# Kernel tuning notes

Measured on AMD Instinct MI355X. Metric: run time of the kernel, lower is better.

Reference implementation:

```python
import jax, jax.numpy as jnp
import numpy as np

B = 16       # graphs per batch
N = 256      # nodes per graph (Hi-C submatrix bins)
NT = B * N   # total nodes
E = 131072   # total edges
DIN = 32     # input feature dim (HYPERPARAMETERS['input_shape'])
H1, H2 = 16, 32
HID = 32     # ContactCNN hidden dim
W7 = 7       # final conv width


def setup_inputs() -> dict:
    key = jax.random.key(0)
    ks = jax.random.split(key, 16)
    x = jax.random.normal(ks[0], (NT, DIN), dtype=jnp.float32)
    edge_index = jax.random.randint(ks[1], (2, E), 0, NT, dtype=jnp.int64)
    edge_attr = jax.random.uniform(ks[2], (E,), dtype=jnp.float32)
    batch_index = jnp.repeat(jnp.arange(B, dtype=jnp.int64), N)
    s = 0.1
    params = dict(
        W0=jax.random.normal(ks[3], (DIN, H1), dtype=jnp.float32) * s,
        b0=jnp.zeros((H1,), dtype=jnp.float32),
        W1=jax.random.normal(ks[4], (H1, H2), dtype=jnp.float32) * s,
        b1=jnp.zeros((H2,), dtype=jnp.float32),
        W2=jax.random.normal(ks[5], (H2, H2), dtype=jnp.float32) * s,
        b2=jnp.zeros((H2,), dtype=jnp.float32),
        Wc=jax.random.normal(ks[6], (HID, H2), dtype=jnp.float32) * s,  # 1x1 conv: [out=HID, in=H2]
        bc=jnp.zeros((HID,), dtype=jnp.float32),
        Wp=jax.random.normal(ks[7], (1, HID, W7, W7), dtype=jnp.float32) * s,  # OIHW
        bp=jnp.zeros((1,), dtype=jnp.float32),
    )
    return dict(x=x, edge_index=edge_index, edge_attr=edge_attr,
                batch_index=batch_index, **params)


def _gcn_norm(edge_index, edge_weight, n):
    # PyG gcn_norm with improved=True (self-loop fill value 2.0)
    src, dst = edge_index[0], edge_index[1]
    loop = jnp.arange(n, dtype=src.dtype)
    src_a = jnp.concatenate([src, loop])
    dst_a = jnp.concatenate([dst, loop])
    w_a = jnp.concatenate([edge_weight, jnp.full((n,), 2.0, dtype=edge_weight.dtype)])
    deg = jax.ops.segment_sum(w_a, dst_a, num_segments=n)
    deg_safe = jnp.where(deg > 0, deg, 1.0)
    dinv = jnp.where(deg > 0, jax.lax.rsqrt(deg_safe), 0.0)
    norm = dinv[src_a] * w_a * dinv[dst_a]
    return src_a, dst_a, norm


def _gcn_layer(h, W, b, src_a, dst_a, norm, n):
    h = h @ W                                  # [n, out]
    msg = norm[:, None] * h[src_a]             # gather + scale
    return jax.ops.segment_sum(msg, dst_a, num_segments=n) + b  # scatter-add


def reference(x, edge_index, edge_attr, batch_index,
              W0, b0, W1, b1, W2, b2, Wc, bc, Wp, bp):
    n = x.shape[0]
    src_a, dst_a, norm = _gcn_norm(edge_index, edge_attr, n)
    h = jax.nn.relu(_gcn_layer(x, W0, b0, src_a, dst_a, norm, n))
    h = jax.nn.relu(_gcn_layer(h, W1, b1, src_a, dst_a, norm, n))
    h = jax.nn.relu(_gcn_layer(h, W2, b2, src_a, dst_a, norm, n))
    z = h.reshape(B, N, -1)                    # process_graph_batch
    # ContactCNN: broadcast outer product -> 1x1 conv -> ReLU -> 7x7 conv -> sigmoid
    zm = jnp.einsum('bid,bjd->bdij', z, z)     # [B, D, N, N]
    c = jax.nn.relu(jnp.einsum('bdij,hd->bhij', zm, Wc) + bc[None, :, None, None])
    s = jax.lax.conv_general_dilated(
        c, Wp, window_strides=(1, 1), padding='SAME',
        dimension_numbers=('NCHW', 'OIHW', 'NCHW')) + bp[None, :, None, None]
    return jax.nn.sigmoid(s)                   # [B, 1, N, N]
```

## Files before the change

kernel.cpp:

```cpp
#include <hip/hip_runtime.h>
#include <hip/hip_bf16.h>
#include <hip/hip_fp16.h>

#define NT 4096
#define NE 131072

#define OFF_DEG  0
#define OFF_A    16384
#define OFF_G1T  33570816
#define OFF_G2T  33701888
#define OFF_G3T  33964032
#define OFF_H3   34226176
#define OFF_W2T  34488320

typedef __attribute__((ext_vector_type(8))) short bf16x8;
typedef __attribute__((ext_vector_type(4))) float f32x4;

__device__ inline unsigned int align16(unsigned int hi, unsigned int lo) {
#if __has_builtin(__builtin_amdgcn_alignbit)
    return __builtin_amdgcn_alignbit(hi, lo, 16);
#else
    return (lo >> 16) | (hi << 16);
#endif
}

__device__ inline unsigned short bfb(float x) {
    return __hip_bfloat16_raw(__float2bfloat16(x)).x;
}

__device__ inline void atomic_add_bf16(unsigned short* base, unsigned int idx, float v) {
    unsigned long long addr = (unsigned long long)(base + (idx & ~1u));
    unsigned int bits = ((unsigned int)bfb(v)) << ((idx & 1u) * 16);
    asm volatile("global_atomic_pk_add_bf16 %0, %1, off" :: "v"(addr), "v"(bits) : "memory");
}


__global__ void k_deg(const int* __restrict__ ei, const float* __restrict__ ew,
                      float* __restrict__ deg) {
    int e = blockIdx.x * 256 + threadIdx.x;
    if (e < NE) atomicAdd(&deg[ei[NE + e]], ew[e]);
}

__global__ void k_scatter(const int* __restrict__ ei, const float* __restrict__ ew,
                          const float* __restrict__ deg, unsigned short* __restrict__ A16,
                          const float* __restrict__ x, const float* __restrict__ W0,
                          unsigned short* __restrict__ G1T,
                          const float* __restrict__ Wp, unsigned int* __restrict__ w2) {
    int e = blockIdx.x * 256 + threadIdx.x;
    if (e < NE) {
        int s = ei[e], d = ei[NE + e];
        float v = rsqrtf(deg[s] + 2.f) * ew[e] * rsqrtf(deg[d] + 2.f);
        atomic_add_bf16(A16, (unsigned int)d * 4096u + (unsigned int)s, v);
    }
    if (e < NT) {
        atomic_add_bf16(A16, (unsigned int)e * 4097u, 2.f / (deg[e] + 2.f));
    }
    if (e < NT * 16) {
        int node = e & 4095, co = e >> 12;
        const float4* xr = (const float4*)(x + node * 32);
        float a = 0.f;
        #pragma unroll
        for (int r = 0; r < 8; r++) {
            float4 f = xr[r];
            a += f.x * W0[(r*4+0)*16 + co] + f.y * W0[(r*4+1)*16 + co]
               + f.z * W0[(r*4+2)*16 + co] + f.w * W0[(r*4+3)*16 + co];
        }
        G1T[co * 4096 + node] = bfb(a);
    }
    if (e >= NE - 1568) {
        int k = e - (NE - 1568);
        __half hh = __float2half(Wp[k]);
        __half2 h2 = __halves2half2(hh, hh);
        w2[k] = *(unsigned int*)&h2;
    }
}


template <int NIN, int NOUT, bool LAST>
__global__ __launch_bounds__(512) void k_gcn(const unsigned short* __restrict__ A16,
                                             const unsigned short* __restrict__ Gt,
                                             const float* __restrict__ bias,
                                             const float* __restrict__ W,
                                             unsigned short* __restrict__ Gout) {
    constexpr int T = NIN / 16;
    __shared__ float red[8][T][16][16];
    __shared__ unsigned short wtile[16 * 40];
    int mt = blockIdx.x;
    int tid = threadIdx.x;
    int w = tid >> 6, lane = tid & 63, m = lane & 15, q = lane >> 4;
    int kw = w * 512;

    const unsigned short* arow = A16 + (size_t)(mt * 16 + m) * 4096 + kw + q * 8;
    f32x4 acc[T];
    #pragma unroll
    for (int t = 0; t < T; t++) acc[t] = (f32x4){0.f, 0.f, 0.f, 0.f};

    bf16x8 wfrag;
    if (!LAST && w < NOUT / 16) {
        #pragma unroll
        for (int j = 0; j < 8; j++) {
            int ci = q * 8 + j;
            wfrag[j] = (ci < NIN) ? (short)bfb(W[ci * NOUT + w * 16 + m]) : (short)0;
        }
    }

    #pragma unroll 4
    for (int s = 0; s < 16; s++) {
        bf16x8 bA = *(const bf16x8*)(arow + s * 32);
        #pragma unroll
        for (int t = 0; t < T; t++) {
            bf16x8 af = *(const bf16x8*)(Gt + (size_t)(t * 16 + m) * 4096 + kw + q * 8 + s * 32);
            acc[t] = __builtin_amdgcn_mfma_f32_16x16x32_bf16(af, bA, acc[t], 0, 0, 0);
        }
    }
    #pragma unroll
    for (int t = 0; t < T; t++)
        #pragma unroll
        for (int r = 0; r < 4; r++) red[w][t][q*4 + r][m] = acc[t][r];
    __syncthreads();

    if (tid < T * 256) {
        int dstp = tid & 15, cop = (tid >> 4) & 15, t = tid >> 8;
        float sum = 0.f;
        #pragma unroll
        for (int w8 = 0; w8 < 8; w8++) sum += red[w8][t][cop][dstp];
        int co = t * 16 + cop;
        float val = fmaxf(sum + bias[co], 0.f);
        if (LAST) Gout[(size_t)(mt * 16 + dstp) * 32 + co] = bfb(val);
        else      wtile[dstp * 40 + co] = bfb(val);
    }
    if (!LAST && NIN == 16 && tid >= 256 && tid < 512) {
        int idx = tid - 256;
        wtile[(idx & 15) * 40 + 16 + ((idx >> 4) & 15)] = 0;
    }
    __syncthreads();

    if (!LAST && w < NOUT / 16) {
        bf16x8 af = *(const bf16x8*)&wtile[m * 40 + q * 8];
        f32x4 o = (f32x4){0.f, 0.f, 0.f, 0.f};
        o = __builtin_amdgcn_mfma_f32_16x16x32_bf16(af, wfrag, o, 0, 0, 0);
        uint2 ov;
        ov.x = (unsigned int)bfb(o[0]) | ((unsigned int)bfb(o[1]) << 16);
        ov.y = (unsigned int)bfb(o[2]) | ((unsigned int)bfb(o[3]) << 16);
        *(uint2*)&Gout[(size_t)(w * 16 + m) * 4096 + mt * 16 + q * 4] = ov;
    }
}


__global__ __launch_bounds__(512) void k_cc(const unsigned short* __restrict__ h3,
                                            const float* __restrict__ Wc,
                                            const float* __restrict__ bc,
                                            const unsigned int* __restrict__ w2,
                                            const float* __restrict__ bp,
                                            float* __restrict__ out) {
    __shared__ unsigned short zs[256 * 40];
    __shared__ float wcs[32 * 36];
    __shared__ __align__(16) unsigned short ct[4 * 32 * 272];
    __shared__ __align__(16) unsigned short pt[4][4096];

    int band = blockIdx.x, bb = blockIdx.y;
    int i0 = band * 16;
    int tid = threadIdx.x;
    int lane = tid & 63, w = tid >> 6;
    int m = lane & 15, q = lane >> 4;

    {
        int row = tid >> 1, half = tid & 1;
        const uint4* src = (const uint4*)(h3 + (size_t)(bb * 256 + row) * 32) + half * 2;
        uint4 v0 = src[0], v1 = src[1];
        uint4* dst = (uint4*)&zs[row * 40 + half * 16];
        dst[0] = v0; dst[1] = v1;
    }
    #pragma unroll
    for (int k = tid; k < 1024; k += 512) wcs[(k >> 5) * 36 + (k & 31)] = Wc[k];
    for (int k = tid; k < 4 * 32 * 136; k += 512) ((unsigned int*)ct)[k] = 0;
    __syncthreads();

    bf16x8 bt[2];
    bool wok[2];
    #pragma unroll
    for (int nt = 0; nt < 2; nt++) {
        int r = i0 - 3 + nt * 16 + m;
        wok[nt] = (unsigned)r < 256u;
        r = r < 0 ? 0 : (r > 255 ? 255 : r);
        bt[nt] = *(const bf16x8*)&zs[r * 40 + q * 8];
    }
    float zaf[2][8];
    #pragma unroll
    for (int jt2 = 0; jt2 < 2; jt2++) {
        bf16x8 za = *(const bf16x8*)&zs[((w * 2 + jt2) * 16 + m) * 40 + q * 8];
        #pragma unroll
        for (int e = 0; e < 8; e++)
            zaf[jt2][e] = __uint_as_float(((unsigned int)(unsigned short)za[e]) << 16);
    }

    int gg = tid >> 7, tx = tid & 31, ty = (tid >> 5) & 3;
    __half2 acc[4][4];
    __half2 zh = __float2half2_rn(0.f);
    #pragma unroll
    for (int o = 0; o < 4; o++)
        #pragma unroll
        for (int p = 0; p < 4; p++) acc[o][p] = zh;

    for (int it = 0; it < 8; it++) {
        #pragma unroll
        for (int g = 0; g < 4; g++) {
            int h = it * 4 + g;
            float wf[8];
            *(float4*)&wf[0] = *(const float4*)&wcs[h * 36 + q * 8];
            *(float4*)&wf[4] = *(const float4*)&wcs[h * 36 + q * 8 + 4];
            float bch = bc[h];
            #pragma unroll
            for (int jt2 = 0; jt2 < 2; jt2++) {
                bf16x8 afv;
                #pragma unroll
                for (int e = 0; e < 8; e++) afv[e] = (short)bfb(zaf[jt2][e] * wf[e]);
                int pos = 4 + (w * 2 + jt2) * 16 + q * 4;
                #pragma unroll
                for (int nt = 0; nt < 2; nt++) {
                    f32x4 d = (f32x4){0.f, 0.f, 0.f, 0.f};
                    d = __builtin_amdgcn_mfma_f32_16x16x32_bf16(afv, bt[nt], d, 0, 0, 0);
                    if (wok[nt]) {
                        float v0 = fmaxf(d[0] + bch, 0.f);
                        float v1 = fmaxf(d[1] + bch, 0.f);
                        float v2 = fmaxf(d[2] + bch, 0.f);
                        float v3 = fmaxf(d[3] + bch, 0.f);
                        __half2 h0 = __floats2half2_rn(v0, v1);
                        __half2 h1 = __floats2half2_rn(v2, v3);
                        uint2 o2;
                        o2.x = *(unsigned int*)&h0;
                        o2.y = *(unsigned int*)&h1;
                        *(uint2*)&ct[g * 8704 + (nt * 16 + m) * 272 + pos] = o2;
                    }
                }
            }
        }
        __syncthreads();

        {
            const unsigned short* C = ct + gg * 8704;
            const __half2* wrow = (const __half2*)w2 + (it * 4 + gg) * 49;
            #pragma unroll
            for (int dr = 0; dr < 10; dr++) {
                const uint4* p4 = (const uint4*)&C[(ty * 4 + dr) * 272 + tx * 8];
                uint4 ua = p4[0], ub = p4[1];
                unsigned int E[8] = {ua.x, ua.y, ua.z, ua.w, ub.x, ub.y, ub.z, ub.w};
                unsigned int O[7];
                #pragma unroll
                for (int k = 0; k < 7; k++) O[k] = align16(E[k + 1], E[k]);
                #pragma unroll
                for (int o = 0; o < 4; o++) {
                    if (dr - o < 0 || dr - o > 6) continue;
                    int di = dr - o;
                    #pragma unroll
                    for (int dj = 0; dj < 7; dj++) {
                        __half2 wv = wrow[di * 7 + dj];
                        #pragma unroll
                        for (int pr = 0; pr < 4; pr++) {
                            int s = 2 * pr + dj + 1;
                            unsigned int pv = (s & 1) ? O[s >> 1] : E[s >> 1];
                            acc[o][pr] = __hfma2(wv, *(__half2*)&pv, acc[o][pr]);
                        }
                    }
                }
            }
        }
        __syncthreads();
    }

    #pragma unroll
    for (int o = 0; o < 4; o++) {
        uint4 v;
        v.x = *(unsigned int*)&acc[o][0];
        v.y = *(unsigned int*)&acc[o][1];
        v.z = *(unsigned int*)&acc[o][2];
        v.w = *(unsigned int*)&acc[o][3];
        *(uint4*)&pt[gg][(ty * 4 + o) * 256 + tx * 8] = v;
    }
    __syncthreads();

    {
        int base = tid * 8;
        float fs[8];
        #pragma unroll
        for (int e = 0; e < 8; e++) fs[e] = 0.f;
        #pragma unroll
        for (int g = 0; g < 4; g++) {
            uint4 v = *(const uint4*)&pt[g][base];
            unsigned int uu[4] = {v.x, v.y, v.z, v.w};
            #pragma unroll
            for (int d = 0; d < 4; d++) {
                float2 f = __half22float2(*(__half2*)&uu[d]);
                fs[2 * d] += f.x; fs[2 * d + 1] += f.y;
            }
        }
        float bpv = bp[0];
        float rs[8];
        #pragma unroll
        for (int e = 0; e < 8; e++) rs[e] = 1.0f / (1.0f + __expf(-(fs[e] + bpv)));
        int row = base >> 8, col = base & 255;
        float* op = &out[((size_t)(bb * 256) + i0 + row) * 256 + col];
        *(float4*)op = make_float4(rs[0], rs[1], rs[2], rs[3]);
        *(float4*)(op + 4) = make_float4(rs[4], rs[5], rs[6], rs[7]);
    }
}


extern "C" void kernel_launch(void* const* d_in, const int* in_sizes, int n_in,
                              void* d_out, int out_size, void* d_ws, size_t ws_size,
                              hipStream_t stream) {
    const float* x  = (const float*)d_in[0];
    const int*   ei = (const int*)d_in[1];
    const float* ew = (const float*)d_in[2];
    const float* W0 = (const float*)d_in[4];
    const float* b0 = (const float*)d_in[5];
    const float* W1 = (const float*)d_in[6];
    const float* b1 = (const float*)d_in[7];
    const float* W2 = (const float*)d_in[8];
    const float* b2 = (const float*)d_in[9];
    const float* Wc = (const float*)d_in[10];
    const float* bc = (const float*)d_in[11];
    const float* Wp = (const float*)d_in[12];
    const float* bp = (const float*)d_in[13];

    char* ws = (char*)d_ws;
    float*          deg  = (float*)(ws + OFF_DEG);
    unsigned short* A16  = (unsigned short*)(ws + OFF_A);
    unsigned short* G1T  = (unsigned short*)(ws + OFF_G1T);
    unsigned short* G2T  = (unsigned short*)(ws + OFF_G2T);
    unsigned short* G3T  = (unsigned short*)(ws + OFF_G3T);
    unsigned short* H3   = (unsigned short*)(ws + OFF_H3);
    unsigned int*   w2t  = (unsigned int*)(ws + OFF_W2T);

    (void)hipMemsetAsync(d_ws, 0, 16384 + 33554432, stream);

    k_deg    <<<NE/256, 256, 0, stream>>>(ei, ew, deg);
    k_scatter<<<NE/256, 256, 0, stream>>>(ei, ew, deg, A16, x, W0, G1T, Wp, w2t);

    k_gcn<16, 32, false><<<256, 512, 0, stream>>>(A16, G1T, b0, W1, G2T);
    k_gcn<32, 32, false><<<256, 512, 0, stream>>>(A16, G2T, b1, W2, G3T);
    k_gcn<32, 32, true> <<<256, 512, 0, stream>>>(A16, G3T, b2, nullptr, H3);

    k_cc<<<dim3(16, 16), 512, 0, stream>>>(H3, Wc, bc, w2t, bp, (float*)d_out);
}
```

Baseline: 196.5 us.

## Fuse graph-construction and GCN layers into one persistent kernel with grid barriers

Replaces the workspace memset, degree, scatter and three GCN-layer launches with a single persistent kernel of 256 blocks. Stages are separated by software grid barriers built on atomic counters, and the dense adjacency zeroing moves into the kernel itself. The aim is to remove launch gaps and the separate memset pass. In exchange it relies on all 256 blocks being co-resident, since the spin barriers otherwise deadlock, and it adds barrier latency between stages.

Result: slower. 280.8 us (+42.9%).

```diff
diff --git a/kernel.cpp b/kernel.cpp
--- a/kernel.cpp
+++ b/kernel.cpp
@@ -4,6 +4,7 @@
 
 #define NT 4096
 #define NE 131072
+#define NBLK 256
 
 #define OFF_DEG  0
 #define OFF_A    16384
@@ -12,6 +13,7 @@
 #define OFF_G3T  33964032
 #define OFF_H3   34226176
 #define OFF_W2T  34488320
+#define OFF_BAR  34496512
 
 typedef __attribute__((ext_vector_type(8))) short bf16x8;
 typedef __attribute__((ext_vector_type(4))) float f32x4;
@@ -34,59 +36,31 @@
     asm volatile("global_atomic_pk_add_bf16 %0, %1, off" :: "v"(addr), "v"(bits) : "memory");
 }
 
-
-__global__ void k_deg(const int* __restrict__ ei, const float* __restrict__ ew,
-                      float* __restrict__ deg) {
-    int e = blockIdx.x * 256 + threadIdx.x;
-    if (e < NE) atomicAdd(&deg[ei[NE + e]], ew[e]);
-}
-
-__global__ void k_scatter(const int* __restrict__ ei, const float* __restrict__ ew,
-                          const float* __restrict__ deg, unsigned short* __restrict__ A16,
-                          const float* __restrict__ x, const float* __restrict__ W0,
-                          unsigned short* __restrict__ G1T,
-                          const float* __restrict__ Wp, unsigned int* __restrict__ w2) {
-    int e = blockIdx.x * 256 + threadIdx.x;
-    if (e < NE) {
-        int s = ei[e], d = ei[NE + e];
-        float v = rsqrtf(deg[s] + 2.f) * ew[e] * rsqrtf(deg[d] + 2.f);
-        atomic_add_bf16(A16, (unsigned int)d * 4096u + (unsigned int)s, v);
-    }
-    if (e < NT) {
-        atomic_add_bf16(A16, (unsigned int)e * 4097u, 2.f / (deg[e] + 2.f));
-    }
-    if (e < NT * 16) {
-        int node = e & 4095, co = e >> 12;
-        const float4* xr = (const float4*)(x + node * 32);
-        float a = 0.f;
-        #pragma unroll
-        for (int r = 0; r < 8; r++) {
-            float4 f = xr[r];
-            a += f.x * W0[(r*4+0)*16 + co] + f.y * W0[(r*4+1)*16 + co]
-               + f.z * W0[(r*4+2)*16 + co] + f.w * W0[(r*4+3)*16 + co];
-        }
-        G1T[co * 4096 + node] = bfb(a);
-    }
-    if (e >= NE - 1568) {
-        int k = e - (NE - 1568);
-        __half hh = __float2half(Wp[k]);
-        __half2 h2 = __halves2half2(hh, hh);
-        w2[k] = *(unsigned int*)&h2;
-    }
-}
-
+__device__ inline void gbar(unsigned int* ctr) {
+    __syncthreads();
+    if (threadIdx.x == 0) {
+        __threadfence();
+        __hip_atomic_fetch_add(ctr, 1u, __ATOMIC_RELAXED, __HIP_MEMORY_SCOPE_AGENT);
+        while (__hip_atomic_load(ctr, __ATOMIC_RELAXED, __HIP_MEMORY_SCOPE_AGENT) < NBLK)
+            __builtin_amdgcn_s_sleep(2);
+        __threadfence();
+    }
+    __syncthreads();
+}
+
+struct GcnSmem {
+    float red[8][2][16][16];
+    unsigned short wtile[16 * 40];
+};
 
 template <int NIN, int NOUT, bool LAST>
-__global__ __launch_bounds__(512) void k_gcn(const unsigned short* __restrict__ A16,
-                                             const unsigned short* __restrict__ Gt,
-                                             const float* __restrict__ bias,
-                                             const float* __restrict__ W,
-                                             unsigned short* __restrict__ Gout) {
+__device__ inline void gcn_phase(GcnSmem& sm, const unsigned short* __restrict__ A16,
+                                 const unsigned short* __restrict__ Gt,
+                                 const float* __restrict__ bias,
+                                 const float* __restrict__ W,
+                                 unsigned short* __restrict__ Gout,
+                                 int mt, int tid) {
     constexpr int T = NIN / 16;
-    __shared__ float red[8][T][16][16];
-    __shared__ unsigned short wtile[16 * 40];
-    int mt = blockIdx.x;
-    int tid = threadIdx.x;
     int w = tid >> 6, lane = tid & 63, m = lane & 15, q = lane >> 4;
     int kw = w * 512;
 
@@ -116,27 +90,27 @@
     #pragma unroll
     for (int t = 0; t < T; t++)
         #pragma unroll
-        for (int r = 0; r < 4; r++) red[w][t][q*4 + r][m] = acc[t][r];
+        for (int r = 0; r < 4; r++) sm.red[w][t][q * 4 + r][m] = acc[t][r];
     __syncthreads();
 
     if (tid < T * 256) {
         int dstp = tid & 15, cop = (tid >> 4) & 15, t = tid >> 8;
         float sum = 0.f;
         #pragma unroll
-        for (int w8 = 0; w8 < 8; w8++) sum += red[w8][t][cop][dstp];
+        for (int w8 = 0; w8 < 8; w8++) sum += sm.red[w8][t][cop][dstp];
         int co = t * 16 + cop;
         float val = fmaxf(sum + bias[co], 0.f);
         if (LAST) Gout[(size_t)(mt * 16 + dstp) * 32 + co] = bfb(val);
-        else      wtile[dstp * 40 + co] = bfb(val);
+        else      sm.wtile[dstp * 40 + co] = bfb(val);
     }
     if (!LAST && NIN == 16 && tid >= 256 && tid < 512) {
         int idx = tid - 256;
-        wtile[(idx & 15) * 40 + 16 + ((idx >> 4) & 15)] = 0;
+        sm.wtile[(idx & 15) * 40 + 16 + ((idx >> 4) & 15)] = 0;
     }
     __syncthreads();
 
     if (!LAST && w < NOUT / 16) {
-        bf16x8 af = *(const bf16x8*)&wtile[m * 40 + q * 8];
+        bf16x8 af = *(const bf16x8*)&sm.wtile[m * 40 + q * 8];
         f32x4 o = (f32x4){0.f, 0.f, 0.f, 0.f};
         o = __builtin_amdgcn_mfma_f32_16x16x32_bf16(af, wfrag, o, 0, 0, 0);
         uint2 ov;
@@ -144,6 +118,75 @@
         ov.y = (unsigned int)bfb(o[2]) | ((unsigned int)bfb(o[3]) << 16);
         *(uint2*)&Gout[(size_t)(w * 16 + m) * 4096 + mt * 16 + q * 4] = ov;
     }
+    __syncthreads();
+}
+
+__global__ __launch_bounds__(512) void k_graph(
+        const int* __restrict__ ei, const float* __restrict__ ew,
+        const float* __restrict__ x, const float* __restrict__ W0,
+        const float* __restrict__ b0, const float* __restrict__ W1,
+        const float* __restrict__ b1, const float* __restrict__ W2,
+        const float* __restrict__ b2, const float* __restrict__ Wp,
+        unsigned int* __restrict__ w2, float* __restrict__ deg,
+        unsigned short* __restrict__ A16,
+        unsigned short* __restrict__ G1T, unsigned short* __restrict__ G2T,
+        unsigned short* __restrict__ G3T, unsigned short* __restrict__ H3,
+        unsigned int* __restrict__ bars) {
+    __shared__ GcnSmem sm;
+    int blk = blockIdx.x, tid = threadIdx.x;
+    int gid = blk * 512 + tid;
+
+    {
+        uint4 z4 = {0u, 0u, 0u, 0u};
+        uint4* ap = (uint4*)(A16 + (size_t)blk * 16 * 4096);
+        #pragma unroll
+        for (int k = 0; k < 16; k++) ap[tid + k * 512] = z4;
+        if (blk == 0) {
+            float4 zf = {0.f, 0.f, 0.f, 0.f};
+            float4* dp = (float4*)deg;
+            dp[tid * 2] = zf;
+            dp[tid * 2 + 1] = zf;
+        }
+    }
+    gbar(&bars[0]);
+
+    atomicAdd(&deg[ei[NE + gid]], ew[gid]);
+    gbar(&bars[1]);
+
+    {
+        int s = ei[gid], d = ei[NE + gid];
+        float v = rsqrtf(deg[s] + 2.f) * ew[gid] * rsqrtf(deg[d] + 2.f);
+        atomic_add_bf16(A16, (unsigned int)d * 4096u + (unsigned int)s, v);
+        if (gid < NT * 16) {
+            int node = gid & 4095, co = gid >> 12;
+            const float4* xr = (const float4*)(x + node * 32);
+            float a = 0.f;
+            #pragma unroll
+            for (int r = 0; r < 8; r++) {
+                float4 f = xr[r];
+                a += f.x * W0[(r*4+0)*16 + co] + f.y * W0[(r*4+1)*16 + co]
+                   + f.z * W0[(r*4+2)*16 + co] + f.w * W0[(r*4+3)*16 + co];
+            }
+            G1T[co * 4096 + node] = bfb(a);
+        }
+        if (gid >= NT * 16 && gid < NT * 16 + 1568) {
+            int k = gid - NT * 16;
+            __half hh = __float2half(Wp[k]);
+            __half2 h2 = __halves2half2(hh, hh);
+            w2[k] = *(unsigned int*)&h2;
+        }
+        if (gid >= NE - NT) {
+            int n = gid - (NE - NT);
+            atomic_add_bf16(A16, (unsigned int)n * 4097u, 2.f / (deg[n] + 2.f));
+        }
+    }
+    gbar(&bars[2]);
+
+    gcn_phase<16, 32, false>(sm, A16, G1T, b0, W1, G2T, blk, tid);
+    gbar(&bars[3]);
+    gcn_phase<32, 32, false>(sm, A16, G2T, b1, W2, G3T, blk, tid);
+    gbar(&bars[4]);
+    gcn_phase<32, 32, true >(sm, A16, G3T, b2, nullptr, H3, blk, tid);
 }
 
 
@@ -331,15 +374,11 @@
     unsigned short* G3T  = (unsigned short*)(ws + OFF_G3T);
     unsigned short* H3   = (unsigned short*)(ws + OFF_H3);
     unsigned int*   w2t  = (unsigned int*)(ws + OFF_W2T);
-
-    (void)hipMemsetAsync(d_ws, 0, 16384 + 33554432, stream);
-
-    k_deg    <<<NE/256, 256, 0, stream>>>(ei, ew, deg);
-    k_scatter<<<NE/256, 256, 0, stream>>>(ei, ew, deg, A16, x, W0, G1T, Wp, w2t);
-
-    k_gcn<16, 32, false><<<256, 512, 0, stream>>>(A16, G1T, b0, W1, G2T);
-    k_gcn<32, 32, false><<<256, 512, 0, stream>>>(A16, G2T, b1, W2, G3T);
-    k_gcn<32, 32, true> <<<256, 512, 0, stream>>>(A16, G3T, b2, nullptr, H3);
-
+    unsigned int*   bars = (unsigned int*)(ws + OFF_BAR);
+
+    (void)hipMemsetAsync(bars, 0, 64, stream);
+
+    k_graph<<<NBLK, 512, 0, stream>>>(ei, ew, x, W0, b0, W1, b1, W2, b2,
+                                      Wp, w2t, deg, A16, G1T, G2T, G3T, H3, bars);
     k_cc<<<dim3(16, 16), 512, 0, stream>>>(H3, Wc, bc, w2t, bp, (float*)d_out);
 }
```

## Halve contact-CNN row bands and fuse A16 zeroing into degree kernel

Applied to the files above, without the earlier changes.

The contact-CNN kernel now covers 8 output rows per block instead of 16. The grid doubles to 512 blocks, shared buffers shrink and a launch-bounds occupancy hint is added, with each thread now holding a single output row of accumulators. This trades more recomputation of the 7x7 halo rows (the 1x1 conv runs over 16 padded rows for every 8 outputs) for more blocks and higher occupancy on the GPU. Separately, the 32 MB memset of the dense adjacency is folded into the degree atomic kernel as vectorized stores, leaving only a small memset for the degree array.

After: 206.6 us. 5.1% more time.

```diff
diff --git a/kernel.cpp b/kernel.cpp
--- a/kernel.cpp
+++ b/kernel.cpp
@@ -35,10 +35,17 @@
 }
 
 
-__global__ void k_deg(const int* __restrict__ ei, const float* __restrict__ ew,
-                      float* __restrict__ deg) {
-    int e = blockIdx.x * 256 + threadIdx.x;
-    if (e < NE) atomicAdd(&deg[ei[NE + e]], ew[e]);
+__global__ __launch_bounds__(256) void k_zerodeg(const int* __restrict__ ei,
+                                                 const float* __restrict__ ew,
+                                                 float* __restrict__ deg,
+                                                 unsigned short* __restrict__ A16) {
+    int blk = blockIdx.x, tid = threadIdx.x;
+    uint4 z4 = {0u, 0u, 0u, 0u};
+    uint4* ap = (uint4*)(A16 + (size_t)blk * 16384);
+    #pragma unroll
+    for (int k = 0; k < 8; k++) ap[tid + k * 256] = z4;
+    int gid = blk * 256 + tid;
+    if (gid < NE) atomicAdd(&deg[ei[NE + gid]], ew[gid]);
 }
 
 __global__ void k_scatter(const int* __restrict__ ei, const float* __restrict__ ew,
@@ -147,19 +154,19 @@
 }
 
 
-__global__ __launch_bounds__(512) void k_cc(const unsigned short* __restrict__ h3,
-                                            const float* __restrict__ Wc,
-                                            const float* __restrict__ bc,
-                                            const unsigned int* __restrict__ w2,
-                                            const float* __restrict__ bp,
-                                            float* __restrict__ out) {
+__global__ __launch_bounds__(512, 4) void k_cc(const unsigned short* __restrict__ h3,
+                                               const float* __restrict__ Wc,
+                                               const float* __restrict__ bc,
+                                               const unsigned int* __restrict__ w2,
+                                               const float* __restrict__ bp,
+                                               float* __restrict__ out) {
     __shared__ unsigned short zs[256 * 40];
     __shared__ float wcs[32 * 36];
-    __shared__ __align__(16) unsigned short ct[4 * 32 * 272];
-    __shared__ __align__(16) unsigned short pt[4][4096];
+    __shared__ __align__(16) unsigned short ct[2 * 16 * 272];
+    __shared__ __align__(16) unsigned short pt[2][2048];
 
     int band = blockIdx.x, bb = blockIdx.y;
-    int i0 = band * 16;
+    int i0 = band * 8;
     int tid = threadIdx.x;
     int lane = tid & 63, w = tid >> 6;
     int m = lane & 15, q = lane >> 4;
@@ -173,17 +180,16 @@
     }
     #pragma unroll
     for (int k = tid; k < 1024; k += 512) wcs[(k >> 5) * 36 + (k & 31)] = Wc[k];
-    for (int k = tid; k < 4 * 32 * 136; k += 512) ((unsigned int*)ct)[k] = 0;
+    for (int k = tid; k < 2 * 16 * 136; k += 512) ((unsigned int*)ct)[k] = 0;
     __syncthreads();
 
-    bf16x8 bt[2];
-    bool wok[2];
-    #pragma unroll
-    for (int nt = 0; nt < 2; nt++) {
-        int r = i0 - 3 + nt * 16 + m;
-        wok[nt] = (unsigned)r < 256u;
+    bf16x8 bt;
+    bool wok;
+    {
+        int r = i0 - 3 + m;
+        wok = (unsigned)r < 256u;
         r = r < 0 ? 0 : (r > 255 ? 255 : r);
-        bt[nt] = *(const bf16x8*)&zs[r * 40 + q * 8];
+        bt = *(const bf16x8*)&zs[r * 40 + q * 8];
     }
     float zaf[2][8];
     #pragma unroll
@@ -194,18 +200,17 @@
             zaf[jt2][e] = __uint_as_float(((unsigned int)(unsigned short)za[e]) << 16);
     }
 
-    int gg = tid >> 7, tx = tid & 31, ty = (tid >> 5) & 3;
-    __half2 acc[4][4];
+    int gg = tid >> 8, idx = tid & 255;
+    int tx = idx & 31, ty = idx >> 5;
+    __half2 acc[4];
     __half2 zh = __float2half2_rn(0.f);
     #pragma unroll
-    for (int o = 0; o < 4; o++)
-        #pragma unroll
-        for (int p = 0; p < 4; p++) acc[o][p] = zh;
-
-    for (int it = 0; it < 8; it++) {
-        #pragma unroll
-        for (int g = 0; g < 4; g++) {
-            int h = it * 4 + g;
+    for (int p = 0; p < 4; p++) acc[p] = zh;
+
+    for (int it = 0; it < 16; it++) {
+        #pragma unroll
+        for (int g = 0; g < 2; g++) {
+            int h = it * 2 + g;
             float wf[8];
             *(float4*)&wf[0] = *(const float4*)&wcs[h * 36 + q * 8];
             *(float4*)&wf[4] = *(const float4*)&wcs[h * 36 + q * 8 + 4];
@@ -216,51 +221,43 @@
                 #pragma unroll
                 for (int e = 0; e < 8; e++) afv[e] = (short)bfb(zaf[jt2][e] * wf[e]);
                 int pos = 4 + (w * 2 + jt2) * 16 + q * 4;
-                #pragma unroll
-                for (int nt = 0; nt < 2; nt++) {
-                    f32x4 d = (f32x4){0.f, 0.f, 0.f, 0.f};
-                    d = __builtin_amdgcn_mfma_f32_16x16x32_bf16(afv, bt[nt], d, 0, 0, 0);
-                    if (wok[nt]) {
-                        float v0 = fmaxf(d[0] + bch, 0.f);
-                        float v1 = fmaxf(d[1] + bch, 0.f);
-                        float v2 = fmaxf(d[2] + bch, 0.f);
-                        float v3 = fmaxf(d[3] + bch, 0.f);
-                        __half2 h0 = __floats2half2_rn(v0, v1);
-                        __half2 h1 = __floats2half2_rn(v2, v3);
-                        uint2 o2;
-                        o2.x = *(unsigned int*)&h0;
-                        o2.y = *(unsigned int*)&h1;
-                        *(uint2*)&ct[g * 8704 + (nt * 16 + m) * 272 + pos] = o2;
-                    }
+                f32x4 d = (f32x4){0.f, 0.f, 0.f, 0.f};
+                d = __builtin_amdgcn_mfma_f32_16x16x32_bf16(afv, bt, d, 0, 0, 0);
+                if (wok) {
+                    float v0 = fmaxf(d[0] + bch, 0.f);
+                    float v1 = fmaxf(d[1] + bch, 0.f);
+                    float v2 = fmaxf(d[2] + bch, 0.f);
+                    float v3 = fmaxf(d[3] + bch, 0.f);
+                    __half2 h0 = __floats2half2_rn(v0, v1);
+                    __half2 h1 = __floats2half2_rn(v2, v3);
+                    uint2 o2;
+                    o2.x = *(unsigned int*)&h0;
+                    o2.y = *(unsigned int*)&h1;
+                    *(uint2*)&ct[g * 4352 + m * 272 + pos] = o2;
                 }
             }
         }
         __syncthreads();
 
         {
-            const unsigned short* C = ct + gg * 8704;
-            const __half2* wrow = (const __half2*)w2 + (it * 4 + gg) * 49;
+            const unsigned short* C = ct + gg * 4352;
+            const __half2* wrow = (const __half2*)w2 + (it * 2 + gg) * 49;
             #pragma unroll
-            for (int dr = 0; dr < 10; dr++) {
-                const uint4* p4 = (const uint4*)&C[(ty * 4 + dr) * 272 + tx * 8];
+            for (int dr = 0; dr < 7; dr++) {
+                const uint4* p4 = (const uint4*)&C[(ty + dr) * 272 + tx * 8];
                 uint4 ua = p4[0], ub = p4[1];
                 unsigned int E[8] = {ua.x, ua.y, ua.z, ua.w, ub.x, ub.y, ub.z, ub.w};
                 unsigned int O[7];
                 #pragma unroll
                 for (int k = 0; k < 7; k++) O[k] = align16(E[k + 1], E[k]);
                 #pragma unroll
-                for (int o = 0; o < 4; o++) {
-                    if (dr - o < 0 || dr - o > 6) continue;
-                    int di = dr - o;
+                for (int dj = 0; dj < 7; dj++) {
+                    __half2 wv = wrow[dr * 7 + dj];
                     #pragma unroll
-                    for (int dj = 0; dj < 7; dj++) {
-                        __half2 wv = wrow[di * 7 + dj];
-                        #pragma unroll
-                        for (int pr = 0; pr < 4; pr++) {
-                            int s = 2 * pr + dj + 1;
-                            unsigned int pv = (s & 1) ? O[s >> 1] : E[s >> 1];
-                            acc[o][pr] = __hfma2(wv, *(__half2*)&pv, acc[o][pr]);
-                        }
+                    for (int pr = 0; pr < 4; pr++) {
+                        int s = 2 * pr + dj + 1;
+                        unsigned int pv = (s & 1) ? O[s >> 1] : E[s >> 1];
+                        acc[pr] = __hfma2(wv, *(__half2*)&pv, acc[pr]);
                     }
                 }
             }
@@ -268,40 +265,39 @@
         __syncthreads();
     }
 
-    #pragma unroll
-    for (int o = 0; o < 4; o++) {
+    {
         uint4 v;
-        v.x = *(unsigned int*)&acc[o][0];
-        v.y = *(unsigned int*)&acc[o][1];
-        v.z = *(unsigned int*)&acc[o][2];
-        v.w = *(unsigned int*)&acc[o][3];
-        *(uint4*)&pt[gg][(ty * 4 + o) * 256 + tx * 8] = v;
+        v.x = *(unsigned int*)&acc[0];
+        v.y = *(unsigned int*)&acc[1];
+        v.z = *(unsigned int*)&acc[2];
+        v.w = *(unsigned int*)&acc[3];
+        *(uint4*)&pt[gg][ty * 256 + tx * 8] = v;
     }
     __syncthreads();
 
     {
-        int base = tid * 8;
-        float fs[8];
-        #pragma unroll
-        for (int e = 0; e < 8; e++) fs[e] = 0.f;
-        #pragma unroll
-        for (int g = 0; g < 4; g++) {
-            uint4 v = *(const uint4*)&pt[g][base];
-            unsigned int uu[4] = {v.x, v.y, v.z, v.w};
+        int base = tid * 4;
+        float fs[4];
+        #pragma unroll
+        for (int e = 0; e < 4; e++) fs[e] = 0.f;
+        #pragma unroll
+        for (int g = 0; g < 2; g++) {
+            uint2 v = *(const uint2*)&pt[g][base];
+            unsigned int uu[2] = {v.x, v.y};
             #pragma unroll
-            for (int d = 0; d < 4; d++) {
+            for (int d = 0; d < 2; d++) {
                 float2 f = __half22float2(*(__half2*)&uu[d]);
                 fs[2 * d] += f.x; fs[2 * d + 1] += f.y;
             }
         }
         float bpv = bp[0];
-        float rs[8];
-        #pragma unroll
-        for (int e = 0; e < 8; e++) rs[e] = 1.0f / (1.0f + __expf(-(fs[e] + bpv)));
+        float4 r;
+        r.x = 1.0f / (1.0f + __expf(-(fs[0] + bpv)));
+        r.y = 1.0f / (1.0f + __expf(-(fs[1] + bpv)));
+        r.z = 1.0f / (1.0f + __expf(-(fs[2] + bpv)));
+        r.w = 1.0f / (1.0f + __expf(-(fs[3] + bpv)));
         int row = base >> 8, col = base & 255;
-        float* op = &out[((size_t)(bb * 256) + i0 + row) * 256 + col];
-        *(float4*)op = make_float4(rs[0], rs[1], rs[2], rs[3]);
-        *(float4*)(op + 4) = make_float4(rs[4], rs[5], rs[6], rs[7]);
+        *(float4*)&out[((size_t)(bb * 256) + i0 + row) * 256 + col] = r;
     }
 }
 
@@ -332,14 +328,14 @@
     unsigned short* H3   = (unsigned short*)(ws + OFF_H3);
     unsigned int*   w2t  = (unsigned int*)(ws + OFF_W2T);
 
-    (void)hipMemsetAsync(d_ws, 0, 16384 + 33554432, stream);
-
-    k_deg    <<<NE/256, 256, 0, stream>>>(ei, ew, deg);
+    (void)hipMemsetAsync(deg, 0, 16384, stream);
+
+    k_zerodeg<<<1024, 256, 0, stream>>>(ei, ew, deg, A16);
     k_scatter<<<NE/256, 256, 0, stream>>>(ei, ew, deg, A16, x, W0, G1T, Wp, w2t);
 
     k_gcn<16, 32, false><<<256, 512, 0, stream>>>(A16, G1T, b0, W1, G2T);
     k_gcn<32, 32, false><<<256, 512, 0, stream>>>(A16, G2T, b1, W2, G3T);
     k_gcn<32, 32, true> <<<256, 512, 0, stream>>>(A16, G3T, b2, nullptr, H3);
 
-    k_cc<<<dim3(16, 16), 512, 0, stream>>>(H3, Wc, bc, w2t, bp, (float*)d_out);
-}
+    k_cc<<<dim3(32, 16), 512, 0, stream>>>(H3, Wc, bc, w2t, bp, (float*)d_out);
+}
```
